# Optimization experiments

Measured on AMD Instinct MI355X. Metric: run time of the kernel, lower is better.

Reference implementation:

```python
import jax, jax.numpy as jnp
import numpy as np

HID = 512      # hidden_dim
MID = 256      # hid_dim
COND_D = 256   # condition_op_dim
OP_D = 32      # operator_len
EX_D = 32      # extra_info_num
L, N, T = 16, 1024, 8
EPS = 1e-5


def _lstm_cell(x_proj, h, c, Whh, bhh):
    # x_proj: precomputed x @ Wih.T + bih, shape [B, 4H]
    gates = x_proj + h @ Whh.T + bhh
    i, f, g, o = jnp.split(gates, 4, axis=-1)
    i = jax.nn.sigmoid(i); f = jax.nn.sigmoid(f)
    g = jnp.tanh(g); o = jax.nn.sigmoid(o)
    c = f * c + i * g
    h = o * jnp.tanh(c)
    return h, c


def _batchnorm(x, gamma, beta):
    mu = x.mean(0)
    var = x.var(0)  # biased, matches PyTorch training-mode normalization
    return gamma * (x - mu) * jax.lax.rsqrt(var + EPS) + beta


def setup_inputs() -> dict:
    key = jax.random.key(0)
    ks = jax.random.split(key, 24)
    s = lambda *sh: 0.05
    inp = {
        'operators': jax.random.normal(ks[0], (L, N, OP_D), jnp.float32),
        'extra_infos': jax.random.normal(ks[1], (L, N, EX_D), jnp.float32),
        'conditions': jax.random.normal(ks[2], (L, N, T, COND_D), jnp.float32),
        'condition_masks': jnp.ones((L, N, 1), jnp.float32),
        'mapping': jax.random.randint(ks[3], (L, N, 2), 0, N + 1, jnp.int32).astype(jnp.int64),
        'lstm1_Wih': jax.random.normal(ks[4], (4 * HID, COND_D), jnp.float32) * 0.05,
        'lstm1_Whh': jax.random.normal(ks[5], (4 * HID, HID), jnp.float32) * 0.05,
        'lstm1_bih': jnp.zeros((4 * HID,), jnp.float32),
        'lstm1_bhh': jnp.zeros((4 * HID,), jnp.float32),
        'cond_W': jax.random.normal(ks[6], (MID, HID), jnp.float32) * 0.05,
        'cond_b': jnp.zeros((MID,), jnp.float32),
        'bn1_g': jnp.ones((MID,), jnp.float32),
        'bn1_b': jnp.zeros((MID,), jnp.float32),
        'lstm2_Wih': jax.random.normal(ks[7], (4 * HID, OP_D + EX_D + MID), jnp.float32) * 0.05,
        'lstm2_Whh': jax.random.normal(ks[8], (4 * HID, HID), jnp.float32) * 0.05,
        'lstm2_bih': jnp.zeros((4 * HID,), jnp.float32),
        'lstm2_bhh': jnp.zeros((4 * HID,), jnp.float32),
        'bn2_g': jnp.ones((HID,), jnp.float32),
        'bn2_b': jnp.zeros((HID,), jnp.float32),
    }
    return inp


def reference(operators, extra_infos, conditions, condition_masks, mapping,
              lstm1_Wih, lstm1_Whh, lstm1_bih, lstm1_bhh,
              cond_W, cond_b, bn1_g, bn1_b,
              lstm2_Wih, lstm2_Whh, lstm2_bih, lstm2_bhh,
              bn2_g, bn2_b):
    B = L * N
    x = conditions.reshape(B, T, COND_D)
    # lstm1 over conditions; precompute input projections for all steps
    xp = jnp.einsum('btd,gd->btg', x, lstm1_Wih) + lstm1_bih  # [B,T,4H]

    def step1(carry, xt):
        h, c = carry
        h, c = _lstm_cell(xt, h, c, lstm1_Whh, lstm1_bhh)
        return (h, c), None

    h0 = jnp.zeros((B, HID), xp.dtype)
    (h1, _), _ = jax.lax.scan(step1, (h0, h0), jnp.swapaxes(xp, 0, 1))

    last = jax.nn.relu(h1 @ cond_W.T + cond_b)       # [B, MID]
    last = _batchnorm(last, bn1_g, bn1_b).reshape(L, N, MID)

    out = jnp.concatenate([operators, extra_infos, last], axis=2)  # [L,N,IN2]
    xp2 = jnp.einsum('lnd,gd->lng', out, lstm2_Wih) + lstm2_bih    # [L,N,4H]

    hz = jnp.zeros((N, HID), xp2.dtype)
    h, c = _lstm_cell(xp2[L - 1], hz, hz, lstm2_Whh, lstm2_bhh)

    mapping = mapping.astype(jnp.int32)
    levels = jnp.arange(L - 2, -1, -1)

    def tree_step(carry, idx):
        h, c = carry
        mp = mapping[idx]  # [N,2]
        pad = jnp.zeros((1, HID), h.dtype)
        ph = jnp.concatenate([pad, h], 0)  # [N+1,H]
        pc = jnp.concatenate([pad, c], 0)
        h = (ph[mp[:, 0]] + ph[mp[:, 1]]) * 0.5
        c = (pc[mp[:, 0]] + pc[mp[:, 1]]) * 0.5
        h, c = _lstm_cell(xp2[idx], h, c, lstm2_Whh, lstm2_bhh)
        return (h, c), None

    (h, c), _ = jax.lax.scan(tree_step, (h, c), levels)

    # batch_size == N since all operator rows are nonzero
    return _batchnorm(h, bn2_g, bn2_b)  # [N, HID]
```

## Files before the change

### kernel.cpp

```cpp
#include <hip/hip_runtime.h>
#include <hip/hip_bf16.h>
#include <stdint.h>


typedef __bf16 bf16;
typedef __bf16 bf16x8 __attribute__((ext_vector_type(8)));
typedef float f32x4 __attribute__((ext_vector_type(4)));

#define HIDDEN 512

__device__ __forceinline__ float sigmoidf_(float x) { return 1.f / (1.f + __expf(-x)); }

__device__ __forceinline__ void async16(const bf16* g, bf16* l) {
  __builtin_amdgcn_global_load_lds(
      (const __attribute__((address_space(1))) void*)g,
      (__attribute__((address_space(3))) void*)l, 16, 0, 0);
}

__global__ void cvt8(const float* __restrict__ src, bf16* __restrict__ dst) {
  size_t i = ((size_t)blockIdx.x * blockDim.x + threadIdx.x) * 8;
  float4 a = *(const float4*)(src + i);
  float4 b = *(const float4*)(src + i + 4);
  bf16x8 r;
  r[0] = (bf16)a.x; r[1] = (bf16)a.y; r[2] = (bf16)a.z; r[3] = (bf16)a.w;
  r[4] = (bf16)b.x; r[5] = (bf16)b.y; r[6] = (bf16)b.z; r[7] = (bf16)b.w;
  *(bf16x8*)(dst + i) = r;
}

__global__ void detect(const int* __restrict__ map, int* __restrict__ flags) {
  __shared__ int any;
  if (threadIdx.x == 0) any = 0;
  __syncthreads();
  int loc = 0;
  for (int i = threadIdx.x; i < 16384; i += blockDim.x) loc |= map[2 * i + 1];
  if (loc) atomicOr(&any, 1);
  __syncthreads();
  if (threadIdx.x == 0) flags[0] = (any == 0) ? 1 : 0;
}

template <int MT>
__global__ __launch_bounds__(256, 2) void cell_gemm(
    const bf16* __restrict__ A0, int a0off, int a0s, int a0kt,
    const bf16* __restrict__ A1, int a1s, int a1kt,
    const bf16* __restrict__ B0, int b0s,
    const bf16* __restrict__ B1, int b1s,
    const float* __restrict__ bias0, const float* __restrict__ bias1,
    const void* __restrict__ xp_add, int xp_f32,
    const float* __restrict__ c_prev,
    float* __restrict__ c_out,
    bf16* __restrict__ h_b16, float* __restrict__ h_f32)
{
  constexpr int BM = MT * 32;
  __shared__ __align__(16) bf16 sA[BM * 64];
  __shared__ __align__(16) bf16 sB[128 * 64];
  const int tid = threadIdx.x;
  const int lane = tid & 63;
  const int quad = lane >> 4, cl = lane & 15;
  const int wave = tid >> 6;
  const int wr = wave >> 1, wc = wave & 1;
  const int bm0 = blockIdx.x * BM;
  const int j0 = blockIdx.y * 32;

  f32x4 acc[MT][4];
#pragma unroll
  for (int mi = 0; mi < MT; ++mi)
#pragma unroll
    for (int g = 0; g < 4; ++g) acc[mi][g] = f32x4{0.f, 0.f, 0.f, 0.f};

  const int nkt = a0kt + a1kt;
  for (int kt = 0; kt < nkt; ++kt) {
    const bf16* abase; int astr, acol;
    const bf16* bbase; int bstr, bcol;
    if (kt < a0kt) {
      abase = A0; astr = a0s; acol = a0off + kt * 64;
      bbase = B0; bstr = b0s; bcol = kt * 64;
    } else {
      abase = A1; astr = a1s; acol = (kt - a0kt) * 64;
      bbase = B1; bstr = b1s; bcol = (kt - a0kt) * 64;
    }
#pragma unroll
    for (int ia = 0; ia < MT; ++ia) {
      int e = ia * 256 + tid;
      int row = e >> 3, sl = e & 7;
      int src = sl ^ (row & 7);
      async16(abase + (size_t)(bm0 + row) * astr + acol + src * 8, sA + e * 8);
    }
#pragma unroll
    for (int ib = 0; ib < 4; ++ib) {
      int e = ib * 256 + tid;
      int row = e >> 3, sl = e & 7;
      int src = sl ^ (row & 7);
      int wrow = (row >> 5) * HIDDEN + j0 + (row & 31);
      async16(bbase + (size_t)wrow * bstr + bcol + src * 8, sB + e * 8);
    }
    __syncthreads();
#pragma unroll
    for (int kh = 0; kh < 2; ++kh) {
      bf16x8 af[MT], bfr[4];
#pragma unroll
      for (int mi = 0; mi < MT; ++mi) {
        int row = wr * (MT * 16) + mi * 16 + cl;
        int sl = (kh * 4 + quad) ^ (row & 7);
        af[mi] = *(const bf16x8*)&sA[row * 64 + sl * 8];
      }
#pragma unroll
      for (int g = 0; g < 4; ++g) {
        int row = g * 32 + wc * 16 + cl;
        int sl = (kh * 4 + quad) ^ (row & 7);
        bfr[g] = *(const bf16x8*)&sB[row * 64 + sl * 8];
      }
#pragma unroll
      for (int mi = 0; mi < MT; ++mi)
#pragma unroll
        for (int g = 0; g < 4; ++g)
          acc[mi][g] = __builtin_amdgcn_mfma_f32_16x16x32_bf16(af[mi], bfr[g], acc[mi][g], 0, 0, 0);
    }
    __syncthreads();
  }

  const int j = j0 + wc * 16 + cl;
  float bI = 0.f, bF = 0.f, bG = 0.f, bO = 0.f;
  if (bias0) {
    bI += bias0[j]; bF += bias0[HIDDEN + j];
    bG += bias0[2 * HIDDEN + j]; bO += bias0[3 * HIDDEN + j];
  }
  if (bias1) {
    bI += bias1[j]; bF += bias1[HIDDEN + j];
    bG += bias1[2 * HIDDEN + j]; bO += bias1[3 * HIDDEN + j];
  }
#pragma unroll
  for (int mi = 0; mi < MT; ++mi) {
    int rb = bm0 + wr * (MT * 16) + mi * 16 + quad * 4;
#pragma unroll
    for (int r = 0; r < 4; ++r) {
      int row = rb + r;
      float gi = acc[mi][0][r] + bI;
      float gf = acc[mi][1][r] + bF;
      float gg = acc[mi][2][r] + bG;
      float go = acc[mi][3][r] + bO;
      if (xp_add) {
        size_t base = (size_t)row * 2048;
        if (xp_f32) {
          const float* xr = (const float*)xp_add + base;
          gi += xr[j]; gf += xr[HIDDEN + j];
          gg += xr[2 * HIDDEN + j]; go += xr[3 * HIDDEN + j];
        } else {
          const bf16* xr = (const bf16*)xp_add + base;
          gi += (float)xr[j]; gf += (float)xr[HIDDEN + j];
          gg += (float)xr[2 * HIDDEN + j]; go += (float)xr[3 * HIDDEN + j];
        }
      }
      float iv = sigmoidf_(gi), fv = sigmoidf_(gf);
      float gv = tanhf(gg), ov = sigmoidf_(go);
      float cp = c_prev ? c_prev[(size_t)row * HIDDEN + j] : 0.f;
      float cn = fv * cp + iv * gv;
      float hn = ov * tanhf(cn);
      c_out[(size_t)row * HIDDEN + j] = cn;
      if (h_b16) h_b16[(size_t)row * HIDDEN + j] = (bf16)hn;
      if (h_f32) h_f32[(size_t)row * HIDDEN + j] = hn;
    }
  }
}

__global__ __launch_bounds__(256, 2) void plain_gemm(
    const bf16* __restrict__ A0, int a0s, int a0kt,
    const bf16* __restrict__ A1, int a1s, int a1kt,
    const bf16* __restrict__ A2, int a2s, int a2kt,
    const bf16* __restrict__ B, int bs,
    const float* __restrict__ bias, int do_relu,
    bf16* __restrict__ outh, float* __restrict__ outf, int Ntot)
{
  __shared__ __align__(16) bf16 sA[128 * 32];
  __shared__ __align__(16) bf16 sB[128 * 32];
  const int tid = threadIdx.x;
  const int lane = tid & 63;
  const int quad = lane >> 4, cl = lane & 15;
  const int wave = tid >> 6;
  const int wr = wave >> 1, wc = wave & 1;
  const int bm0 = blockIdx.x * 128;
  const int bn0 = blockIdx.y * 128;

  f32x4 acc[4][4];
#pragma unroll
  for (int mi = 0; mi < 4; ++mi)
#pragma unroll
    for (int ni = 0; ni < 4; ++ni) acc[mi][ni] = f32x4{0.f, 0.f, 0.f, 0.f};

  const int nkt = a0kt + a1kt + a2kt;
  for (int kt = 0; kt < nkt; ++kt) {
    const bf16* abase; int astr, acol;
    if (kt < a0kt)            { abase = A0; astr = a0s; acol = kt * 32; }
    else if (kt < a0kt + a1kt){ abase = A1; astr = a1s; acol = (kt - a0kt) * 32; }
    else                      { abase = A2; astr = a2s; acol = (kt - a0kt - a1kt) * 32; }
#pragma unroll
    for (int it = 0; it < 2; ++it) {
      int e = it * 256 + tid;
      int row = e >> 2, sl = e & 3;
      int src = sl ^ ((row >> 1) & 3);
      async16(abase + (size_t)(bm0 + row) * astr + acol + src * 8, sA + e * 8);
      async16(B + (size_t)(bn0 + row) * bs + kt * 32 + src * 8, sB + e * 8);
    }
    __syncthreads();
    bf16x8 af[4], bfr[4];
#pragma unroll
    for (int mi = 0; mi < 4; ++mi) {
      int row = wr * 64 + mi * 16 + cl;
      int sl = quad ^ ((row >> 1) & 3);
      af[mi] = *(const bf16x8*)&sA[row * 32 + sl * 8];
    }
#pragma unroll
    for (int ni = 0; ni < 4; ++ni) {
      int row = wc * 64 + ni * 16 + cl;
      int sl = quad ^ ((row >> 1) & 3);
      bfr[ni] = *(const bf16x8*)&sB[row * 32 + sl * 8];
    }
#pragma unroll
    for (int mi = 0; mi < 4; ++mi)
#pragma unroll
      for (int ni = 0; ni < 4; ++ni)
        acc[mi][ni] = __builtin_amdgcn_mfma_f32_16x16x32_bf16(af[mi], bfr[ni], acc[mi][ni], 0, 0, 0);
    __syncthreads();
  }

#pragma unroll
  for (int mi = 0; mi < 4; ++mi) {
    int rb = bm0 + wr * 64 + mi * 16 + quad * 4;
#pragma unroll
    for (int ni = 0; ni < 4; ++ni) {
      int col = bn0 + wc * 64 + ni * 16 + cl;
      float bv = bias ? bias[col] : 0.f;
#pragma unroll
      for (int r = 0; r < 4; ++r) {
        int row = rb + r;
        float v = acc[mi][ni][r] + bv;
        if (do_relu) v = fmaxf(v, 0.f);
        if (outf) outf[(size_t)row * Ntot + col] = v;
        else      outh[(size_t)row * Ntot + col] = (bf16)v;
      }
    }
  }
}

__global__ void gather_h(const int* __restrict__ map, const int* __restrict__ flags,
                         int level,
                         const float* __restrict__ h_src, const float* __restrict__ c_src,
                         bf16* __restrict__ hA, float* __restrict__ c_dst)
{
  int n = blockIdx.x, t = threadIdx.x;
  long base = (long)level * 2048 + n * 2;
  int m0, m1;
  if (flags[0]) { m0 = map[base * 2]; m1 = map[base * 2 + 2]; }
  else          { m0 = map[base];     m1 = map[base + 1]; }
  float h0 = m0 ? h_src[(size_t)(m0 - 1) * HIDDEN + t] : 0.f;
  float h1 = m1 ? h_src[(size_t)(m1 - 1) * HIDDEN + t] : 0.f;
  float c0 = m0 ? c_src[(size_t)(m0 - 1) * HIDDEN + t] : 0.f;
  float c1 = m1 ? c_src[(size_t)(m1 - 1) * HIDDEN + t] : 0.f;
  hA[(size_t)n * HIDDEN + t] = (bf16)(0.5f * (h0 + h1));
  c_dst[(size_t)n * HIDDEN + t] = 0.5f * (c0 + c1);
}

__global__ void cell0(const void* __restrict__ xp, int xp_f32,
                      const float* __restrict__ bhh,
                      float* __restrict__ h, float* __restrict__ c)
{
  int n = blockIdx.x, j = threadIdx.x;
  float g[4];
#pragma unroll
  for (int k = 0; k < 4; ++k) {
    size_t idx = (size_t)n * 2048 + k * 512 + j;
    float v = xp_f32 ? ((const float*)xp)[idx] : (float)((const bf16*)xp)[idx];
    g[k] = v + bhh[k * 512 + j];
  }
  float cv = sigmoidf_(g[0]) * tanhf(g[2]);
  h[(size_t)n * HIDDEN + j] = sigmoidf_(g[3]) * tanhf(cv);
  c[(size_t)n * HIDDEN + j] = cv;
}

__global__ void bn_reduce_b16(const bf16* __restrict__ x, int rpb, int F,
                              float* __restrict__ partials) {
  int col = threadIdx.x, b = blockIdx.x;
  const bf16* p = x + (size_t)b * rpb * F + col;
  float s = 0.f, q = 0.f;
  for (int r = 0; r < rpb; ++r) { float v = (float)p[(size_t)r * F]; s += v; q += v * v; }
  partials[(size_t)b * 2 * F + col] = s;
  partials[(size_t)b * 2 * F + F + col] = q;
}

__global__ void bn_reduce_f32(const float* __restrict__ x, int rpb, int F,
                              float* __restrict__ partials) {
  int col = threadIdx.x, b = blockIdx.x;
  const float* p = x + (size_t)b * rpb * F + col;
  float s = 0.f, q = 0.f;
  for (int r = 0; r < rpb; ++r) { float v = p[(size_t)r * F]; s += v; q += v * v; }
  partials[(size_t)b * 2 * F + col] = s;
  partials[(size_t)b * 2 * F + F + col] = q;
}

__global__ void bn_final(const float* __restrict__ partials, int nb, int F,
                         const float* __restrict__ g, const float* __restrict__ b,
                         float invB, float* __restrict__ scale, float* __restrict__ shift) {
  int j = threadIdx.x;
  float s = 0.f, q = 0.f;
  for (int i = 0; i < nb; ++i) {
    s += partials[(size_t)i * 2 * F + j];
    q += partials[(size_t)i * 2 * F + F + j];
  }
  float mu = s * invB;
  float var = fmaxf(q * invB - mu * mu, 0.f);
  float sc = g[j] * rsqrtf(var + 1e-5f);
  scale[j] = sc;
  shift[j] = b[j] - sc * mu;
}

__global__ void bn_apply_mid(const bf16* __restrict__ x, const float* __restrict__ scale,
                             const float* __restrict__ shift, int Fmask, size_t total,
                             bf16* __restrict__ out) {
  for (size_t i = blockIdx.x * (size_t)blockDim.x + threadIdx.x; i < total;
       i += (size_t)gridDim.x * blockDim.x) {
    int j = (int)(i & (size_t)Fmask);
    out[i] = (bf16)(scale[j] * (float)x[i] + shift[j]);
  }
}

__global__ void bn_apply_out(const float* __restrict__ x, const float* __restrict__ scale,
                             const float* __restrict__ shift, int Fmask, size_t total,
                             float* __restrict__ out) {
  for (size_t i = blockIdx.x * (size_t)blockDim.x + threadIdx.x; i < total;
       i += (size_t)gridDim.x * blockDim.x) {
    int j = (int)(i & (size_t)Fmask);
    out[i] = scale[j] * x[i] + shift[j];
  }
}

extern "C" void kernel_launch(void* const* d_in, const int* in_sizes, int n_in,
                              void* d_out, int out_size, void* d_ws, size_t ws_size,
                              hipStream_t stream) {
  const float* operators = (const float*)d_in[0];
  const float* extras    = (const float*)d_in[1];
  const float* conds     = (const float*)d_in[2];
  const int*   mapping   = (const int*)d_in[4];
  const float* b1ih = (const float*)d_in[7];
  const float* b1hh = (const float*)d_in[8];
  const float* condb = (const float*)d_in[10];
  const float* bn1g = (const float*)d_in[11];
  const float* bn1b = (const float*)d_in[12];
  const float* b2ih = (const float*)d_in[15];
  const float* b2hh = (const float*)d_in[16];
  const float* bn2g = (const float*)d_in[17];
  const float* bn2b = (const float*)d_in[18];

  char* ws = (char*)d_ws;
  size_t o = 0;
  auto alloc = [&](size_t bytes) {
    char* p = ws + o;
    o += (bytes + 255) & ~(size_t)255;
    return p;
  };
  bf16* conds_b = (bf16*)alloc((size_t)33554432 * 2);
  bf16* ops_b   = (bf16*)alloc((size_t)524288 * 2);
  bf16* ext_b   = (bf16*)alloc((size_t)524288 * 2);
  bf16* w1ih_b  = (bf16*)alloc((size_t)524288 * 2);
  bf16* w1hh_b  = (bf16*)alloc((size_t)1048576 * 2);
  bf16* condw_b = (bf16*)alloc((size_t)131072 * 2);
  bf16* w2ih_b  = (bf16*)alloc((size_t)655360 * 2);
  bf16* w2hh_b  = (bf16*)alloc((size_t)1048576 * 2);
  bf16* h1[2];
  h1[0] = (bf16*)alloc((size_t)16384 * 512 * 2);
  h1[1] = (bf16*)alloc((size_t)16384 * 512 * 2);
  float* c1 = (float*)alloc((size_t)16384 * 512 * 4);
  bf16* last_relu = (bf16*)alloc((size_t)16384 * 256 * 2);
  bf16* last_bn = (bf16*)alloc((size_t)16384 * 256 * 2);
  float* h2 = (float*)alloc((size_t)1024 * 512 * 4);
  bf16* hA = (bf16*)alloc((size_t)1024 * 512 * 2);
  float* c2a = (float*)alloc((size_t)1024 * 512 * 4);
  float* c2b = (float*)alloc((size_t)1024 * 512 * 4);
  float* partials = (float*)alloc((size_t)64 * 1024 * 4);
  float* scale1 = (float*)alloc(256 * 4);
  float* shift1 = (float*)alloc(256 * 4);
  float* scale2 = (float*)alloc(512 * 4);
  float* shift2 = (float*)alloc(512 * 4);
  int* flags = (int*)alloc(256);

  size_t xp2_elems = (size_t)16384 * 2048;
  int xpf = (o + xp2_elems * 4 <= ws_size) ? 1 : 0;
  void* xp2 = alloc(xp2_elems * (xpf ? 4 : 2));
  float* xp2f = xpf ? (float*)xp2 : nullptr;
  bf16* xp2h = xpf ? nullptr : (bf16*)xp2;

  detect<<<1, 256, 0, stream>>>(mapping, flags);
  cvt8<<<16384, 256, 0, stream>>>(conds, conds_b);
  cvt8<<<256, 256, 0, stream>>>(operators, ops_b);
  cvt8<<<256, 256, 0, stream>>>(extras, ext_b);
  cvt8<<<256, 256, 0, stream>>>((const float*)d_in[5], w1ih_b);
  cvt8<<<512, 256, 0, stream>>>((const float*)d_in[6], w1hh_b);
  cvt8<<<64, 256, 0, stream>>>((const float*)d_in[9], condw_b);
  cvt8<<<320, 256, 0, stream>>>((const float*)d_in[13], w2ih_b);
  cvt8<<<512, 256, 0, stream>>>((const float*)d_in[14], w2hh_b);

  for (int t = 0; t < 8; ++t) {
    const bf16* hprev = (t == 0) ? nullptr : h1[t & 1];
    cell_gemm<4><<<dim3(128, 16), 256, 0, stream>>>(
        conds_b, t * 256, 2048, 4,
        hprev, 512, (t == 0) ? 0 : 8,
        w1ih_b, 256, w1hh_b, 512,
        b1ih, b1hh,
        nullptr, 0,
        (t == 0) ? nullptr : c1, c1, h1[(t + 1) & 1], nullptr);
  }

  plain_gemm<<<dim3(128, 2), 256, 0, stream>>>(
      h1[0], 512, 16, nullptr, 0, 0, nullptr, 0, 0,
      condw_b, 512, condb, 1, last_relu, nullptr, 256);
  bn_reduce_b16<<<64, 256, 0, stream>>>(last_relu, 256, 256, partials);
  bn_final<<<1, 256, 0, stream>>>(partials, 64, 256, bn1g, bn1b, 1.f / 16384.f, scale1, shift1);
  bn_apply_mid<<<1024, 256, 0, stream>>>(last_relu, scale1, shift1, 255,
                                         (size_t)16384 * 256, last_bn);

  plain_gemm<<<dim3(128, 16), 256, 0, stream>>>(
      ops_b, 32, 1, ext_b, 32, 1, last_bn, 256, 8,
      w2ih_b, 320, b2ih, 0, xp2h, xp2f, 2048);

  size_t lvl_sz = (size_t)1024 * 2048;
  const void* xp15 = xpf ? (const void*)(xp2f + 15 * lvl_sz) : (const void*)(xp2h + 15 * lvl_sz);
  cell0<<<1024, 512, 0, stream>>>(xp15, xpf, b2hh, h2, c2a);
  for (int idx = 14; idx >= 0; --idx) {
    gather_h<<<1024, 512, 0, stream>>>(mapping, flags, idx, h2, c2a, hA, c2b);
    const void* xpl = xpf ? (const void*)(xp2f + idx * lvl_sz) : (const void*)(xp2h + idx * lvl_sz);
    cell_gemm<2><<<dim3(16, 16), 256, 0, stream>>>(
        hA, 0, 512, 8,
        nullptr, 0, 0,
        w2hh_b, 512, nullptr, 0,
        b2hh, nullptr,
        xpl, xpf,
        c2b, c2a, nullptr, h2);
  }

  bn_reduce_f32<<<16, 512, 0, stream>>>(h2, 64, 512, partials);
  bn_final<<<1, 512, 0, stream>>>(partials, 16, 512, bn2g, bn2b, 1.f / 1024.f, scale2, shift2);
  bn_apply_out<<<512, 256, 0, stream>>>(h2, scale2, shift2, 511,
                                        (size_t)1024 * 512, (float*)d_out);
}
```

Measured before the change: 1.304 ms.

## Fuse tree gather into LSTM cell GEMM and enlarge LSTM1 tile

```diff
diff --git a/kernel.cpp b/kernel.cpp
--- a/kernel.cpp
+++ b/kernel.cpp
@@ -9,7 +9,11 @@
 
 #define HIDDEN 512
 
-__device__ __forceinline__ float sigmoidf_(float x) { return 1.f / (1.f + __expf(-x)); }
+__device__ __forceinline__ float fast_sig(float x) { return 1.f / (1.f + __expf(-x)); }
+__device__ __forceinline__ float fast_tanh(float x) {
+  float e = __expf(2.f * x);
+  return 1.f - 2.f / (e + 1.f);
+}
 
 __device__ __forceinline__ void async16(const bf16* g, bf16* l) {
   __builtin_amdgcn_global_load_lds(
@@ -45,10 +49,9 @@
     const bf16* __restrict__ B0, int b0s,
     const bf16* __restrict__ B1, int b1s,
     const float* __restrict__ bias0, const float* __restrict__ bias1,
-    const void* __restrict__ xp_add, int xp_f32,
     const float* __restrict__ c_prev,
     float* __restrict__ c_out,
-    bf16* __restrict__ h_b16, float* __restrict__ h_f32)
+    bf16* __restrict__ h_b16)
 {
   constexpr int BM = MT * 32;
   __shared__ __align__(16) bf16 sA[BM * 64];
@@ -67,23 +70,139 @@
 #pragma unroll
     for (int g = 0; g < 4; ++g) acc[mi][g] = f32x4{0.f, 0.f, 0.f, 0.f};
 
-  const int nkt = a0kt + a1kt;
-  for (int kt = 0; kt < nkt; ++kt) {
-    const bf16* abase; int astr, acol;
-    const bf16* bbase; int bstr, bcol;
-    if (kt < a0kt) {
-      abase = A0; astr = a0s; acol = a0off + kt * 64;
-      bbase = B0; bstr = b0s; bcol = kt * 64;
-    } else {
-      abase = A1; astr = a1s; acol = (kt - a0kt) * 64;
-      bbase = B1; bstr = b1s; bcol = (kt - a0kt) * 64;
-    }
-#pragma unroll
-    for (int ia = 0; ia < MT; ++ia) {
-      int e = ia * 256 + tid;
+#pragma unroll
+  for (int ph = 0; ph < 2; ++ph) {
+    const int kts = (ph == 0) ? a0kt : a1kt;
+    const bf16* ab = (ph == 0) ? A0 : A1;
+    const int as = (ph == 0) ? a0s : a1s;
+    const int ao = (ph == 0) ? a0off : 0;
+    const bf16* bb = (ph == 0) ? B0 : B1;
+    const int bs = (ph == 0) ? b0s : b1s;
+    for (int kt = 0; kt < kts; ++kt) {
+#pragma unroll
+      for (int ia = 0; ia < MT; ++ia) {
+        int e = ia * 256 + tid;
+        int row = e >> 3, sl = e & 7;
+        int src = sl ^ (row & 7);
+        async16(ab + (size_t)(bm0 + row) * as + ao + kt * 64 + src * 8, sA + e * 8);
+      }
+#pragma unroll
+      for (int ib = 0; ib < 4; ++ib) {
+        int e = ib * 256 + tid;
+        int row = e >> 3, sl = e & 7;
+        int src = sl ^ (row & 7);
+        int wrow = (row >> 5) * HIDDEN + j0 + (row & 31);
+        async16(bb + (size_t)wrow * bs + kt * 64 + src * 8, sB + e * 8);
+      }
+      __syncthreads();
+#pragma unroll
+      for (int kh = 0; kh < 2; ++kh) {
+        bf16x8 af[MT], bfr[4];
+#pragma unroll
+        for (int mi = 0; mi < MT; ++mi) {
+          int row = wr * (MT * 16) + mi * 16 + cl;
+          int sl = (kh * 4 + quad) ^ (row & 7);
+          af[mi] = *(const bf16x8*)&sA[row * 64 + sl * 8];
+        }
+#pragma unroll
+        for (int g = 0; g < 4; ++g) {
+          int row = g * 32 + wc * 16 + cl;
+          int sl = (kh * 4 + quad) ^ (row & 7);
+          bfr[g] = *(const bf16x8*)&sB[row * 64 + sl * 8];
+        }
+#pragma unroll
+        for (int mi = 0; mi < MT; ++mi)
+#pragma unroll
+          for (int g = 0; g < 4; ++g)
+            acc[mi][g] = __builtin_amdgcn_mfma_f32_16x16x32_bf16(af[mi], bfr[g], acc[mi][g], 0, 0, 0);
+      }
+      __syncthreads();
+    }
+  }
+
+  const int j = j0 + wc * 16 + cl;
+  float bI = bias0[j], bF = bias0[HIDDEN + j];
+  float bG = bias0[2 * HIDDEN + j], bO = bias0[3 * HIDDEN + j];
+  if (bias1) {
+    bI += bias1[j]; bF += bias1[HIDDEN + j];
+    bG += bias1[2 * HIDDEN + j]; bO += bias1[3 * HIDDEN + j];
+  }
+#pragma unroll
+  for (int mi = 0; mi < MT; ++mi) {
+    int rb = bm0 + wr * (MT * 16) + mi * 16 + quad * 4;
+#pragma unroll
+    for (int r = 0; r < 4; ++r) {
+      int row = rb + r;
+      float iv = fast_sig(acc[mi][0][r] + bI);
+      float fv = fast_sig(acc[mi][1][r] + bF);
+      float gv = fast_tanh(acc[mi][2][r] + bG);
+      float ov = fast_sig(acc[mi][3][r] + bO);
+      float cp = c_prev ? c_prev[(size_t)row * HIDDEN + j] : 0.f;
+      float cn = fv * cp + iv * gv;
+      float hn = ov * fast_tanh(cn);
+      c_out[(size_t)row * HIDDEN + j] = cn;
+      h_b16[(size_t)row * HIDDEN + j] = (bf16)hn;
+    }
+  }
+}
+
+__global__ __launch_bounds__(256, 2) void cell_tree(
+    const int* __restrict__ map, const int* __restrict__ flags, int level,
+    const bf16* __restrict__ h_src,
+    const float* __restrict__ c_src,
+    const bf16* __restrict__ W,
+    const float* __restrict__ bhh,
+    const void* __restrict__ xp, int xp_f32,
+    float* __restrict__ c_out,
+    bf16* __restrict__ h_out_b,
+    float* __restrict__ h_out_f)
+{
+  __shared__ __align__(16) bf16 sA[64 * 64];
+  __shared__ __align__(16) bf16 sB[128 * 64];
+  __shared__ int smap[128];
+  const int tid = threadIdx.x;
+  const int lane = tid & 63;
+  const int quad = lane >> 4, cl = lane & 15;
+  const int wave = tid >> 6;
+  const int wr = wave >> 1, wc = wave & 1;
+  const int bm0 = blockIdx.x * 64;
+  const int j0 = blockIdx.y * 32;
+
+  if (tid < 128) {
+    long base = (long)level * 2048 + (bm0 + (tid >> 1)) * 2 + (tid & 1);
+    smap[tid] = flags[0] ? map[base * 2] : map[base];
+  }
+  __syncthreads();
+
+  f32x4 acc[2][4];
+#pragma unroll
+  for (int mi = 0; mi < 2; ++mi)
+#pragma unroll
+    for (int g = 0; g < 4; ++g) acc[mi][g] = f32x4{0.f, 0.f, 0.f, 0.f};
+
+  for (int kt = 0; kt < 8; ++kt) {
+#pragma unroll
+    for (int it = 0; it < 2; ++it) {
+      int e = it * 256 + tid;
       int row = e >> 3, sl = e & 7;
       int src = sl ^ (row & 7);
-      async16(abase + (size_t)(bm0 + row) * astr + acol + src * 8, sA + e * 8);
+      int m0 = smap[row * 2], m1 = smap[row * 2 + 1];
+      int col = kt * 64 + src * 8;
+      float a8[8] = {0.f, 0.f, 0.f, 0.f, 0.f, 0.f, 0.f, 0.f};
+      if (m0) {
+        bf16x8 x = *(const bf16x8*)&h_src[(size_t)(m0 - 1) * HIDDEN + col];
+#pragma unroll
+        for (int q = 0; q < 8; ++q) a8[q] += (float)x[q];
+      }
+      if (m1) {
+        bf16x8 x = *(const bf16x8*)&h_src[(size_t)(m1 - 1) * HIDDEN + col];
+#pragma unroll
+        for (int q = 0; q < 8; ++q) a8[q] += (float)x[q];
+      }
+      bf16x8 rr;
+#pragma unroll
+      for (int q = 0; q < 8; ++q) rr[q] = (bf16)(0.5f * a8[q]);
+      *(bf16x8*)&sA[e * 8] = rr;
     }
 #pragma unroll
     for (int ib = 0; ib < 4; ++ib) {
@@ -91,15 +210,15 @@
       int row = e >> 3, sl = e & 7;
       int src = sl ^ (row & 7);
       int wrow = (row >> 5) * HIDDEN + j0 + (row & 31);
-      async16(bbase + (size_t)wrow * bstr + bcol + src * 8, sB + e * 8);
+      async16(W + (size_t)wrow * HIDDEN + kt * 64 + src * 8, sB + e * 8);
     }
     __syncthreads();
 #pragma unroll
     for (int kh = 0; kh < 2; ++kh) {
-      bf16x8 af[MT], bfr[4];
-#pragma unroll
-      for (int mi = 0; mi < MT; ++mi) {
-        int row = wr * (MT * 16) + mi * 16 + cl;
+      bf16x8 af[2], bfr[4];
+#pragma unroll
+      for (int mi = 0; mi < 2; ++mi) {
+        int row = wr * 32 + mi * 16 + cl;
         int sl = (kh * 4 + quad) ^ (row & 7);
         af[mi] = *(const bf16x8*)&sA[row * 64 + sl * 8];
       }
@@ -110,7 +229,7 @@
         bfr[g] = *(const bf16x8*)&sB[row * 64 + sl * 8];
       }
 #pragma unroll
-      for (int mi = 0; mi < MT; ++mi)
+      for (int mi = 0; mi < 2; ++mi)
 #pragma unroll
         for (int g = 0; g < 4; ++g)
           acc[mi][g] = __builtin_amdgcn_mfma_f32_16x16x32_bf16(af[mi], bfr[g], acc[mi][g], 0, 0, 0);
@@ -119,45 +238,39 @@
   }
 
   const int j = j0 + wc * 16 + cl;
-  float bI = 0.f, bF = 0.f, bG = 0.f, bO = 0.f;
-  if (bias0) {
-    bI += bias0[j]; bF += bias0[HIDDEN + j];
-    bG += bias0[2 * HIDDEN + j]; bO += bias0[3 * HIDDEN + j];
-  }
-  if (bias1) {
-    bI += bias1[j]; bF += bias1[HIDDEN + j];
-    bG += bias1[2 * HIDDEN + j]; bO += bias1[3 * HIDDEN + j];
-  }
-#pragma unroll
-  for (int mi = 0; mi < MT; ++mi) {
-    int rb = bm0 + wr * (MT * 16) + mi * 16 + quad * 4;
+  float bI = bhh[j], bF = bhh[HIDDEN + j];
+  float bG = bhh[2 * HIDDEN + j], bO = bhh[3 * HIDDEN + j];
+#pragma unroll
+  for (int mi = 0; mi < 2; ++mi) {
+    int lr0 = wr * 32 + mi * 16 + quad * 4;
 #pragma unroll
     for (int r = 0; r < 4; ++r) {
-      int row = rb + r;
+      int lr = lr0 + r;
+      int row = bm0 + lr;
       float gi = acc[mi][0][r] + bI;
       float gf = acc[mi][1][r] + bF;
       float gg = acc[mi][2][r] + bG;
       float go = acc[mi][3][r] + bO;
-      if (xp_add) {
-        size_t base = (size_t)row * 2048;
-        if (xp_f32) {
-          const float* xr = (const float*)xp_add + base;
-          gi += xr[j]; gf += xr[HIDDEN + j];
-          gg += xr[2 * HIDDEN + j]; go += xr[3 * HIDDEN + j];
-        } else {
-          const bf16* xr = (const bf16*)xp_add + base;
-          gi += (float)xr[j]; gf += (float)xr[HIDDEN + j];
-          gg += (float)xr[2 * HIDDEN + j]; go += (float)xr[3 * HIDDEN + j];
-        }
-      }
-      float iv = sigmoidf_(gi), fv = sigmoidf_(gf);
-      float gv = tanhf(gg), ov = sigmoidf_(go);
-      float cp = c_prev ? c_prev[(size_t)row * HIDDEN + j] : 0.f;
-      float cn = fv * cp + iv * gv;
-      float hn = ov * tanhf(cn);
+      size_t base = (size_t)row * 2048;
+      if (xp_f32) {
+        const float* xr = (const float*)xp + base;
+        gi += xr[j]; gf += xr[HIDDEN + j];
+        gg += xr[2 * HIDDEN + j]; go += xr[3 * HIDDEN + j];
+      } else {
+        const bf16* xr = (const bf16*)xp + base;
+        gi += (float)xr[j]; gf += (float)xr[HIDDEN + j];
+        gg += (float)xr[2 * HIDDEN + j]; go += (float)xr[3 * HIDDEN + j];
+      }
+      int m0 = smap[lr * 2], m1 = smap[lr * 2 + 1];
+      float cp = 0.f;
+      if (m0) cp += c_src[(size_t)(m0 - 1) * HIDDEN + j];
+      if (m1) cp += c_src[(size_t)(m1 - 1) * HIDDEN + j];
+      cp *= 0.5f;
+      float cn = fast_sig(gf) * cp + fast_sig(gi) * fast_tanh(gg);
+      float hn = fast_sig(go) * fast_tanh(cn);
       c_out[(size_t)row * HIDDEN + j] = cn;
-      if (h_b16) h_b16[(size_t)row * HIDDEN + j] = (bf16)hn;
-      if (h_f32) h_f32[(size_t)row * HIDDEN + j] = hn;
+      h_out_b[(size_t)row * HIDDEN + j] = (bf16)hn;
+      if (h_out_f) h_out_f[(size_t)row * HIDDEN + j] = hn;
     }
   }
 }
@@ -241,27 +354,9 @@
   }
 }
 
-__global__ void gather_h(const int* __restrict__ map, const int* __restrict__ flags,
-                         int level,
-                         const float* __restrict__ h_src, const float* __restrict__ c_src,
-                         bf16* __restrict__ hA, float* __restrict__ c_dst)
-{
-  int n = blockIdx.x, t = threadIdx.x;
-  long base = (long)level * 2048 + n * 2;
-  int m0, m1;
-  if (flags[0]) { m0 = map[base * 2]; m1 = map[base * 2 + 2]; }
-  else          { m0 = map[base];     m1 = map[base + 1]; }
-  float h0 = m0 ? h_src[(size_t)(m0 - 1) * HIDDEN + t] : 0.f;
-  float h1 = m1 ? h_src[(size_t)(m1 - 1) * HIDDEN + t] : 0.f;
-  float c0 = m0 ? c_src[(size_t)(m0 - 1) * HIDDEN + t] : 0.f;
-  float c1 = m1 ? c_src[(size_t)(m1 - 1) * HIDDEN + t] : 0.f;
-  hA[(size_t)n * HIDDEN + t] = (bf16)(0.5f * (h0 + h1));
-  c_dst[(size_t)n * HIDDEN + t] = 0.5f * (c0 + c1);
-}
-
 __global__ void cell0(const void* __restrict__ xp, int xp_f32,
                       const float* __restrict__ bhh,
-                      float* __restrict__ h, float* __restrict__ c)
+                      bf16* __restrict__ h, float* __restrict__ c)
 {
   int n = blockIdx.x, j = threadIdx.x;
   float g[4];
@@ -271,8 +366,8 @@
     float v = xp_f32 ? ((const float*)xp)[idx] : (float)((const bf16*)xp)[idx];
     g[k] = v + bhh[k * 512 + j];
   }
-  float cv = sigmoidf_(g[0]) * tanhf(g[2]);
-  h[(size_t)n * HIDDEN + j] = sigmoidf_(g[3]) * tanhf(cv);
+  float cv = fast_sig(g[0]) * fast_tanh(g[2]);
+  h[(size_t)n * HIDDEN + j] = (bf16)(fast_sig(g[3]) * fast_tanh(cv));
   c[(size_t)n * HIDDEN + j] = cv;
 }
 
@@ -370,10 +465,13 @@
   float* c1 = (float*)alloc((size_t)16384 * 512 * 4);
   bf16* last_relu = (bf16*)alloc((size_t)16384 * 256 * 2);
   bf16* last_bn = (bf16*)alloc((size_t)16384 * 256 * 2);
-  float* h2 = (float*)alloc((size_t)1024 * 512 * 4);
-  bf16* hA = (bf16*)alloc((size_t)1024 * 512 * 2);
-  float* c2a = (float*)alloc((size_t)1024 * 512 * 4);
-  float* c2b = (float*)alloc((size_t)1024 * 512 * 4);
+  bf16* h2b[2];
+  h2b[0] = (bf16*)alloc((size_t)1024 * 512 * 2);
+  h2b[1] = (bf16*)alloc((size_t)1024 * 512 * 2);
+  float* c2[2];
+  c2[0] = (float*)alloc((size_t)1024 * 512 * 4);
+  c2[1] = (float*)alloc((size_t)1024 * 512 * 4);
+  float* h2f = (float*)alloc((size_t)1024 * 512 * 4);
   float* partials = (float*)alloc((size_t)64 * 1024 * 4);
   float* scale1 = (float*)alloc(256 * 4);
   float* shift1 = (float*)alloc(256 * 4);
@@ -399,13 +497,12 @@
 
   for (int t = 0; t < 8; ++t) {
     const bf16* hprev = (t == 0) ? nullptr : h1[t & 1];
-    cell_gemm<4><<<dim3(128, 16), 256, 0, stream>>>(
+    cell_gemm<8><<<dim3(64, 16), 256, 0, stream>>>(
         conds_b, t * 256, 2048, 4,
         hprev, 512, (t == 0) ? 0 : 8,
         w1ih_b, 256, w1hh_b, 512,
         b1ih, b1hh,
-        nullptr, 0,
-        (t == 0) ? nullptr : c1, c1, h1[(t + 1) & 1], nullptr);
+        (t == 0) ? nullptr : c1, c1, h1[(t + 1) & 1]);
   }
 
   plain_gemm<<<dim3(128, 2), 256, 0, stream>>>(
@@ -422,21 +519,22 @@
 
   size_t lvl_sz = (size_t)1024 * 2048;
   const void* xp15 = xpf ? (const void*)(xp2f + 15 * lvl_sz) : (const void*)(xp2h + 15 * lvl_sz);
-  cell0<<<1024, 512, 0, stream>>>(xp15, xpf, b2hh, h2, c2a);
+  cell0<<<1024, 512, 0, stream>>>(xp15, xpf, b2hh, h2b[0], c2[0]);
+  int cur = 0;
   for (int idx = 14; idx >= 0; --idx) {
-    gather_h<<<1024, 512, 0, stream>>>(mapping, flags, idx, h2, c2a, hA, c2b);
     const void* xpl = xpf ? (const void*)(xp2f + idx * lvl_sz) : (const void*)(xp2h + idx * lvl_sz);
-    cell_gemm<2><<<dim3(16, 16), 256, 0, stream>>>(
-        hA, 0, 512, 8,
-        nullptr, 0, 0,
-        w2hh_b, 512, nullptr, 0,
-        b2hh, nullptr,
+    cell_tree<<<dim3(16, 16), 256, 0, stream>>>(
+        mapping, flags, idx,
+        h2b[cur], c2[cur],
+        w2hh_b, b2hh,
         xpl, xpf,
-        c2b, c2a, nullptr, h2);
-  }
-
-  bn_reduce_f32<<<16, 512, 0, stream>>>(h2, 64, 512, partials);
+        c2[cur ^ 1], h2b[cur ^ 1],
+        (idx == 0) ? h2f : nullptr);
+    cur ^= 1;
+  }
+
+  bn_reduce_f32<<<16, 512, 0, stream>>>(h2f, 64, 512, partials);
   bn_final<<<1, 512, 0, stream>>>(partials, 16, 512, bn2g, bn2b, 1.f / 1024.f, scale2, shift2);
-  bn_apply_out<<<512, 256, 0, stream>>>(h2, scale2, shift2, 511,
+  bn_apply_out<<<512, 256, 0, stream>>>(h2f, scale2, shift2, 511,
                                         (size_t)1024 * 512, (float*)d_out);
 }
```

Measured after the change: 1.417 ms. +8.7%, slower.
